# Optimization experiments

Hardware: AMD Instinct MI355X
Metric: run time of the kernel (lower is better)

Reference implementation:

```python
import jax, jax.numpy as jnp
import numpy as np
import math

LMAX = 3
NCHAN = 32
NEDGE = 50000

# ---------- Wigner 3j (real spherical-harmonic basis), replicating e3nn ----------

def _su2_cg(j1, j2, j3):
    f = math.factorial
    def coeff(m1, m2, m3):
        vmin = int(max(-j1 + j2 + m3, -j1 + m1, 0))
        vmax = int(min(j2 + j3 + m1, j3 - j1 + j2, j3 + m3))
        C = ((2 * j3 + 1) * f(j3 + j1 - j2) * f(j3 - j1 + j2) * f(j1 + j2 - j3) / f(j1 + j2 + j3 + 1)) ** 0.5
        C *= (f(j3 + m3) * f(j3 - m3) * f(j1 - m1) * f(j1 + m1) * f(j2 - m2) * f(j2 + m2)) ** 0.5
        S = 0.0
        for v in range(vmin, vmax + 1):
            S += (-1.0) ** (v + j2 + m2) * f(j2 + j3 + m1 - v) * f(j1 - m1 + v) / (
                f(v) * f(j3 - j1 + j2 - v) * f(j3 + m3 - v) * f(v + j1 - j2 - m3))
        return C * S
    out = np.zeros((2 * j1 + 1, 2 * j2 + 1, 2 * j3 + 1))
    for m1 in range(-j1, j1 + 1):
        for m2 in range(-j2, j2 + 1):
            m3 = m1 + m2
            if -j3 <= m3 <= j3:
                out[m1 + j1, m2 + j2, m3 + j3] = coeff(m1, m2, m3)
    return out

def _q_real_to_complex(l):
    q = np.zeros((2 * l + 1, 2 * l + 1), dtype=np.complex128)
    for m in range(-l, 0):
        q[l + m, l + abs(m)] = 1 / 2 ** 0.5
        q[l + m, l - abs(m)] = -1j / 2 ** 0.5
    q[l, l] = 1.0
    for m in range(1, l + 1):
        q[l + m, l + abs(m)] = (-1) ** m / 2 ** 0.5
        q[l + m, l - abs(m)] = 1j * (-1) ** m / 2 ** 0.5
    return (-1j) ** l * q

def _wigner_3j(l1, l2, l3):
    C = _su2_cg(l1, l2, l3).astype(np.complex128)
    Q1, Q2, Q3 = _q_real_to_complex(l1), _q_real_to_complex(l2), _q_real_to_complex(l3)
    C = np.einsum('ij,kl,mn,ikn->jlm', Q1, Q2, np.conj(Q3.T), C)
    C = np.real(C)
    return C / np.linalg.norm(C)

# ---------- Instruction enumeration (matches the torch module's __init__) ----------

def _build_paths():
    ls = list(range(LMAX + 1))  # irreps 0e,1o,2e,3o -> parity (-1)^l
    ins = []
    for l1 in ls:
        for l2 in ls:
            for l3 in range(abs(l1 - l2), min(l1 + l2, LMAX) + 1):
                if (l1 + l2 + l3) % 2 == 0:  # parity selection p1*p2 == p3
                    ins.append((l1, l2, l3))
    # e3nn Irreps.sort: stable sort of output blocks by ir; pos[i] = sorted position
    order_sorted = sorted(range(len(ins)), key=lambda i: ins[i][2])
    pos = [0] * len(ins)
    for new, old in enumerate(order_sorted):
        pos[old] = new
    # replicate `outputs.insert(ins.i_out, output)` over instruction iteration order
    concat = []
    for idx in range(len(ins)):
        concat.insert(min(pos[idx], len(concat)), idx)
    offs = np.cumsum([0] + [2 * l + 1 for l in ls]).tolist()  # block offsets in dim-16 layout
    # path_weight: component normalization, one path per output block -> sqrt(2*l3+1)
    cg = [jnp.asarray((_wigner_3j(l1, l2, l3) * math.sqrt(2 * l3 + 1)).astype(np.float32))
          for (l1, l2, l3) in ins]
    return ins, pos, concat, offs, cg

_INS, _POS, _CONCAT, _OFFS, _CG = _build_paths()  # 23 instructions, out dim 99


def setup_inputs() -> dict:
    key = jax.random.key(0)
    k1, k2, k3 = jax.random.split(key, 3)
    x = jax.random.normal(k1, (NEDGE, NCHAN, 16), dtype=jnp.float32)
    y = jax.random.normal(k2, (NEDGE, 1, 16), dtype=jnp.float32)
    weights = jax.random.normal(k3, (NEDGE, len(_INS) * NCHAN, 1), dtype=jnp.float32)
    return {"x": x, "y": y, "weights": weights}


def reference(x, y, weights):
    # x: [E, C, 16], y: [E, 1, 16], weights: [E, n_ins*C, 1]
    C = x.shape[1]
    y2 = y[:, 0, :]  # [E, 16]
    outs = [None] * len(_INS)
    for idx, (l1, l2, l3) in enumerate(_INS):
        o1, o2 = _OFFS[l1], _OFFS[l2]
        xb = x[:, :, o1:o1 + 2 * l1 + 1]            # [E, C, 2l1+1]
        yb = y2[:, o2:o2 + 2 * l2 + 1]              # [E, 2l2+1]
        w = weights[:, _POS[idx] * C:(_POS[idx] + 1) * C, 0]  # [E, C]
        # dense CG contraction == sparse gather-multiply-index_add over (mu1,mu2,mu3)
        blk = jnp.einsum('eci,ej,ijk->eck', xb, yb, _CG[idx])  # [E, C, 2l3+1]
        outs[idx] = w[:, :, None] * blk
    return jnp.concatenate([outs[i] for i in _CONCAT], axis=-1)  # [E, C, 99]
```

## Files before the change

kernel.cpp:

```cpp
#include <hip/hip_runtime.h>
#include <math.h>

#define NPATH 23
#define NEDGE 50000
#define NCHAN 32
#define NWROW 736
#define OUTW  99
#define TTOT  439
#define EPB   2
#define NTHR  256

constexpr int L1[NPATH]    = {0,0,0,0,1,1,1,1,1,1,2,2,2,2,2,2,2,3,3,3,3,3,3};
constexpr int L2[NPATH]    = {0,1,2,3,0,1,1,2,2,3,0,1,1,2,2,3,3,0,1,2,2,3,3};
constexpr int L3[NPATH]    = {0,1,2,3,1,0,2,1,3,2,2,1,3,0,2,1,3,3,2,1,3,0,2};
constexpr int POS[NPATH]   = {0,4,10,17,5,1,11,6,18,12,13,7,19,2,14,8,20,21,15,9,22,3,16};
constexpr int OOFF[NPATH]  = {0,4,7,12,19,1,34,22,39,46,51,31,61,2,73,25,78,85,68,28,92,3,56};
constexpr int TOFF[NPATH]  = {0,1,4,9,16,25,28,43,52,73,88,113,128,163,168,193,208,243,292,327,348,397,404};
constexpr int LOFF[4]      = {0,1,4,9};

constexpr unsigned GMASK4[4] = {0xE0010u, 0x700100u, 0x7C00u, 0x182EFu};

typedef _Float16 __attribute__((ext_vector_type(4))) h4;

__device__ __forceinline__ int imx(int a, int b){ return a > b ? a : b; }
__device__ __forceinline__ int imn(int a, int b){ return a < b ? a : b; }

__device__ __forceinline__ double factd(int n){
    double r = 1.0;
    for(int i = 2; i <= n; ++i) r *= (double)i;
    return r;
}

__global__ __launch_bounds__(512) void cg_setup(float* __restrict__ cgd2){
    const int p  = blockIdx.x;
    const int j1 = L1[p], j2 = L2[p], j3 = L3[p];
    const int n1 = 2*j1+1, n2 = 2*j2+1, n3 = 2*j3+1;
    const int o2 = LOFF[j2];
    const int ntot = n1*n2*n3;
    const int t = threadIdx.x;

    __shared__ double scg[343];
    __shared__ double qre[3][49];
    __shared__ double qim[3][49];
    __shared__ double red[512];

    if(t < ntot){
        int a   = t / (n2*n3);
        int rem = t - a*(n2*n3);
        int b   = rem / n3;
        int g   = rem - b*n3;
        int m1 = a - j1, m2 = b - j2, m3 = g - j3;
        double val = 0.0;
        if(m1 + m2 == m3){
            int vmin = imx(imx(-j1 + j2 + m3, -j1 + m1), 0);
            int vmax = imn(imn(j2 + j3 + m1, j3 - j1 + j2), j3 + m3);
            double C = sqrt((2.0*j3 + 1.0) * factd(j3 + j1 - j2) * factd(j3 - j1 + j2)
                            * factd(j1 + j2 - j3) / factd(j1 + j2 + j3 + 1));
            C *= sqrt(factd(j3 + m3) * factd(j3 - m3) * factd(j1 - m1)
                      * factd(j1 + m1) * factd(j2 - m2) * factd(j2 + m2));
            double S = 0.0;
            for(int v = vmin; v <= vmax; ++v){
                double sgn = ((v + j2 + m2) & 1) ? -1.0 : 1.0;
                S += sgn * factd(j2 + j3 + m1 - v) * factd(j1 - m1 + v)
                     / (factd(v) * factd(j3 - j1 + j2 - v) * factd(j3 + m3 - v)
                        * factd(v + j1 - j2 - m3));
            }
            val = C * S;
        }
        scg[t] = val;
    }

    if(t < 3){
        int l = (t == 0) ? j1 : ((t == 1) ? j2 : j3);
        int n = 2*l + 1;
        double* QR = qre[t];
        double* QI = qim[t];
        for(int i = 0; i < 49; ++i){ QR[i] = 0.0; QI[i] = 0.0; }
        const double is2 = 0.70710678118654752440;
        for(int m = -l; m < 0; ++m){
            QR[(l+m)*n + (l-m)] = is2;
            QI[(l+m)*n + (l+m)] = -is2;
        }
        QR[l*n + l] = 1.0;
        for(int m = 1; m <= l; ++m){
            double s = (m & 1) ? -1.0 : 1.0;
            QR[(l+m)*n + (l+m)] = s * is2;
            QI[(l+m)*n + (l-m)] = s * is2;
        }
        double fr, fi;
        switch(l & 3){
            case 0: fr = 1.0;  fi = 0.0;  break;
            case 1: fr = 0.0;  fi = -1.0; break;
            case 2: fr = -1.0; fi = 0.0;  break;
            default: fr = 0.0; fi = 1.0;  break;
        }
        for(int i = 0; i < n*n; ++i){
            double re = QR[i], im = QI[i];
            QR[i] = re*fr - im*fi;
            QI[i] = re*fi + im*fr;
        }
    }
    __syncthreads();

    double val = 0.0;
    if(t < ntot){
        int j   = t / (n2*n3);
        int rem = t - j*(n2*n3);
        int lq  = rem / n3;
        int m   = rem - lq*n3;
        double acc = 0.0;
        for(int i = 0; i < n1; ++i){
            double q1r = qre[0][i*n1 + j], q1i = qim[0][i*n1 + j];
            if(q1r == 0.0 && q1i == 0.0) continue;
            for(int k = 0; k < n2; ++k){
                double q2r = qre[1][k*n2 + lq], q2i = qim[1][k*n2 + lq];
                if(q2r == 0.0 && q2i == 0.0) continue;
                double ar = q1r*q2r - q1i*q2i;
                double ai = q1r*q2i + q1i*q2r;
                for(int n = 0; n < n3; ++n){
                    double cv = scg[(i*n2 + k)*n3 + n];
                    if(cv == 0.0) continue;
                    double q3r = qre[2][n*n3 + m];
                    double q3i = -qim[2][n*n3 + m];
                    acc += cv * (ar*q3r - ai*q3i);
                }
            }
        }
        val = acc;
    }

    red[t] = val * val;
    __syncthreads();
    if(t < 343) scg[t] = val;
    for(int s2 = 256; s2 > 0; s2 >>= 1){
        if(t < s2) red[t] += red[t + s2];
        __syncthreads();
    }
    const double scale = sqrt(2.0*j3 + 1.0) / sqrt(red[0]);

    for(int u = t; u < n1*n3*16; u += 512){
        int sl = u >> 4, jf = u & 15;
        int i  = sl / n3, k = sl - i*n3;
        int j  = jf - o2;
        double v2 = (j >= 0 && j < n2) ? scg[(i*n2 + j)*n3 + k] : 0.0;
        cgd2[(size_t)(TOFF[p] + sl)*16 + jf] = (float)(v2 * scale);
    }
}

template<int G>
__device__ __forceinline__ void prefetchW(const float* __restrict__ wbase,
                                          float* __restrict__ wreg)
{
    constexpr unsigned mask = GMASK4[G];
    #pragma unroll
    for(int p = 0; p < NPATH; ++p){
        if((mask >> p) & 1u)
            wreg[__builtin_popcount(mask & ((1u << p) - 1u))] = wbase[POS[p]*NCHAN];
    }
}

template<int G>
__device__ __forceinline__ void phaseC(const float* __restrict__ xr,
                                       const float* __restrict__ wreg,
                                       const float* __restrict__ Te,
                                       _Float16* __restrict__ ob)
{
    constexpr unsigned mask = GMASK4[G];
    #pragma unroll
    for(int p = 0; p < NPATH; ++p){
        if(!((mask >> p) & 1u)) continue;
        const int widx = __builtin_popcount(mask & ((1u << p) - 1u));
        const int n1 = 2*L1[p] + 1;
        const int n3 = 2*L3[p] + 1;
        const int o1 = LOFF[L1[p]];
        const float wp = wreg[widx];
        const float* Tp = Te + TOFF[p];
        #pragma unroll
        for(int k = 0; k < n3; ++k){
            float acc = 0.f;
            #pragma unroll
            for(int i = 0; i < n1; ++i)
                acc = fmaf(xr[o1 + i], Tp[i*n3 + k], acc);
            ob[OOFF[p] + k] = (_Float16)(wp * acc);
        }
    }
}

__global__ __launch_bounds__(NTHR, 6) void tp_main(
    const float* __restrict__ x, const float* __restrict__ y,
    const float* __restrict__ w, const float* __restrict__ cgd2,
    float* __restrict__ out)
{
    __shared__ __align__(16) _Float16 obuf[EPB*NCHAN*OUTW];
    __shared__ float Ts[EPB*TTOT];
    __shared__ float ys[EPB*16];

    const int tid = threadIdx.x;
    const int e0  = blockIdx.x * EPB;

    const int c   = tid & 31;
    const int el  = (tid >> 5) & 1;
    const int grp = tid >> 6;
    const int e   = e0 + el;

    const float4* xp = reinterpret_cast<const float4*>(x + (size_t)(e*NCHAN + c)*16);
    float4 x0 = xp[0], x1 = xp[1], x2 = xp[2], x3 = xp[3];

    const float* wbase = w + (size_t)e*NWROW + c;
    float wreg[10];
    switch(grp){
        case 0: prefetchW<0>(wbase, wreg); break;
        case 1: prefetchW<1>(wbase, wreg); break;
        case 2: prefetchW<2>(wbase, wreg); break;
        default: prefetchW<3>(wbase, wreg); break;
    }

    if(tid < EPB*16) ys[tid] = y[e0*16 + tid];
    __syncthreads();

    for(int u = tid; u < EPB*TTOT; u += NTHR){
        int eli = u / TTOT;
        int s   = u - eli*TTOT;
        const float* cr = cgd2 + (size_t)s*16;
        float acc = 0.f;
        #pragma unroll
        for(int j = 0; j < 16; ++j)
            acc = fmaf(ys[eli*16 + j], cr[j], acc);
        Ts[u] = acc;
    }
    __syncthreads();

    float xr[16];
    xr[0]=x0.x;  xr[1]=x0.y;  xr[2]=x0.z;  xr[3]=x0.w;
    xr[4]=x1.x;  xr[5]=x1.y;  xr[6]=x1.z;  xr[7]=x1.w;
    xr[8]=x2.x;  xr[9]=x2.y;  xr[10]=x2.z; xr[11]=x2.w;
    xr[12]=x3.x; xr[13]=x3.y; xr[14]=x3.z; xr[15]=x3.w;

    const float* Te = Ts + el*TTOT;
    _Float16* ob = obuf + el*(NCHAN*OUTW) + c*OUTW;

    switch(grp){
        case 0: phaseC<0>(xr, wreg, Te, ob); break;
        case 1: phaseC<1>(xr, wreg, Te, ob); break;
        case 2: phaseC<2>(xr, wreg, Te, ob); break;
        default: phaseC<3>(xr, wreg, Te, ob); break;
    }
    __syncthreads();

    const h4* ob4 = reinterpret_cast<const h4*>(obuf);
    float4* o4 = reinterpret_cast<float4*>(out + (size_t)blockIdx.x * (EPB*NCHAN*OUTW));
    #pragma unroll
    for(int k2 = 0; k2 < 7; ++k2){
        int idx = tid + k2*NTHR;
        if(idx < EPB*NCHAN*OUTW/4){
            h4 hv = ob4[idx];
            float4 fv = { (float)hv[0], (float)hv[1], (float)hv[2], (float)hv[3] };
            o4[idx] = fv;
        }
    }
}

extern "C" void kernel_launch(void* const* d_in, const int* in_sizes, int n_in,
                              void* d_out, int out_size, void* d_ws, size_t ws_size,
                              hipStream_t stream)
{
    const float* x  = (const float*)d_in[0];
    const float* y  = (const float*)d_in[1];
    const float* wt = (const float*)d_in[2];
    float* out = (float*)d_out;
    float* cgd2 = (float*)d_ws;

    cg_setup<<<NPATH, 512, 0, stream>>>(cgd2);
    tp_main<<<NEDGE/EPB, NTHR, 0, stream>>>(x, y, wt, cgd2, out);
}
```

Before: 267.9 us.

## Compute per-wave CG-y tables locally, pad T layout, pair fp16 LDS stores

Rebalances the path-to-wave grouping so each wave builds only the y-contracted CG entries it will itself consume. That removes the block-wide __syncthreads and the staged y in shared memory, leaving a wave-local lgkmcnt wait. The T table is padded to 4 or 8 floats per row so phase C can read it with float4 LDS loads, and fp16 results are written to LDS in pairs. The obuf row stride is padded to 100. The final global write becomes per-element scalar stores instead of aligned float4 stores, which may reduce store efficiency in a bandwidth-bound kernel.

```diff
diff --git a/kernel.cpp b/kernel.cpp
--- a/kernel.cpp
+++ b/kernel.cpp
@@ -18,7 +18,44 @@
 constexpr int TOFF[NPATH]  = {0,1,4,9,16,25,28,43,52,73,88,113,128,163,168,193,208,243,292,327,348,397,404};
 constexpr int LOFF[4]      = {0,1,4,9};
 
-constexpr unsigned GMASK4[4] = {0xE0010u, 0x700100u, 0x7C00u, 0x182EFu};
+constexpr unsigned GMASKS[4] = {0x122028u, 0x211405u, 0x444100u, 0x88AD2u};
+
+constexpr int PAD(int n1){ return n1 <= 3 ? 4 : 8; }
+
+struct PT { int v[NPATH]; int total; };
+constexpr PT make_ptoff(){
+    PT t{}; int a = 0;
+    for(int p = 0; p < NPATH; ++p){ t.v[p] = a; a += (2*L3[p]+1)*PAD(2*L1[p]+1); }
+    t.total = a;
+    return t;
+}
+constexpr PT PTOF = make_ptoff();
+static_assert(PTOF.total == 632, "padded T size");
+#define TSZ 632
+
+struct BTab { unsigned v[4][28]; int cnt[4]; };
+constexpr BTab make_btab(){
+    BTab b{};
+    for(int g = 0; g < 4; ++g){
+        int n = 0;
+        for(int p = 0; p < NPATH; ++p){
+            if(!((GMASKS[g] >> p) & 1u)) continue;
+            int n1 = 2*L1[p]+1, n3 = 2*L3[p]+1;
+            int o2 = LOFF[L2[p]];
+            int q0 = o2 >> 2;
+            for(int k = 0; k < n3; ++k){
+                b.v[g][n++] = (unsigned)(TOFF[p]+k)
+                            | ((unsigned)n3 << 9) | ((unsigned)n1 << 12)
+                            | ((unsigned)(PAD(n1)==8 ? 1 : 0) << 15)
+                            | ((unsigned)(PTOF.v[p] + k*PAD(n1)) << 16)
+                            | ((unsigned)q0 << 26);
+            }
+        }
+        b.cnt[g] = n;
+    }
+    return b;
+}
+constexpr BTab BT = make_btab();
 
 typedef _Float16 __attribute__((ext_vector_type(4))) h4;
 
@@ -151,11 +188,56 @@
 __device__ __forceinline__ void prefetchW(const float* __restrict__ wbase,
                                           float* __restrict__ wreg)
 {
-    constexpr unsigned mask = GMASK4[G];
+    constexpr unsigned mask = GMASKS[G];
     #pragma unroll
     for(int p = 0; p < NPATH; ++p){
         if((mask >> p) & 1u)
             wreg[__builtin_popcount(mask & ((1u << p) - 1u))] = wbase[POS[p]*NCHAN];
+    }
+}
+
+template<int G>
+__device__ __forceinline__ void phaseB(int lane, int e0,
+                                       const float* __restrict__ y,
+                                       const float* __restrict__ cgd2,
+                                       float* __restrict__ TsL)
+{
+    constexpr int E = BT.cnt[G];
+    if(lane < 2*E){
+        const int el  = (lane >= E) ? 1 : 0;
+        const int idx = lane - el*E;
+        const unsigned ent = BT.v[G][idx];
+        const int slot0 = ent & 511;
+        const int n3    = (ent >> 9)  & 7;
+        const int n1    = (ent >> 12) & 7;
+        const int pad8  = (ent >> 15) & 1;
+        const int dst   = (ent >> 16) & 1023;
+        const int q0    = (ent >> 26) & 3;
+
+        const float* yq = y + (size_t)(e0 + el)*16 + q0*4;
+        float4 y0 = *(const float4*)yq;
+        float4 y1 = *(const float4*)(yq + 4);
+
+        float T[8];
+        #pragma unroll
+        for(int i = 0; i < 8; ++i) T[i] = 0.f;
+        #pragma unroll
+        for(int i = 0; i < 7; ++i){
+            if(i < n1){
+                const float* cr = cgd2 + (size_t)(slot0 + i*n3)*16 + q0*4;
+                float4 c0 = *(const float4*)cr;
+                float4 c1 = *(const float4*)(cr + 4);
+                float a;
+                a = fmaf(c0.x, y0.x, 0.f);  a = fmaf(c0.y, y0.y, a);
+                a = fmaf(c0.z, y0.z, a);    a = fmaf(c0.w, y0.w, a);
+                a = fmaf(c1.x, y1.x, a);    a = fmaf(c1.y, y1.y, a);
+                a = fmaf(c1.z, y1.z, a);    a = fmaf(c1.w, y1.w, a);
+                T[i] = a;
+            }
+        }
+        float* d = TsL + el*TSZ + dst;
+        *(float4*)d = float4{T[0], T[1], T[2], T[3]};
+        if(pad8) *((float4*)d + 1) = float4{T[4], T[5], T[6], T[7]};
     }
 }
 
@@ -165,24 +247,54 @@
                                        const float* __restrict__ Te,
                                        _Float16* __restrict__ ob)
 {
-    constexpr unsigned mask = GMASK4[G];
+    constexpr unsigned mask = GMASKS[G];
     #pragma unroll
     for(int p = 0; p < NPATH; ++p){
         if(!((mask >> p) & 1u)) continue;
         const int widx = __builtin_popcount(mask & ((1u << p) - 1u));
-        const int n1 = 2*L1[p] + 1;
-        const int n3 = 2*L3[p] + 1;
-        const int o1 = LOFF[L1[p]];
+        const int n1  = 2*L1[p] + 1;
+        const int n3  = 2*L3[p] + 1;
+        const int o1  = LOFF[L1[p]];
+        const int pad = PAD(n1);
         const float wp = wreg[widx];
-        const float* Tp = Te + TOFF[p];
+
+        float acc[7];
         #pragma unroll
         for(int k = 0; k < n3; ++k){
-            float acc = 0.f;
-            #pragma unroll
-            for(int i = 0; i < n1; ++i)
-                acc = fmaf(xr[o1 + i], Tp[i*n3 + k], acc);
-            ob[OOFF[p] + k] = (_Float16)(wp * acc);
-        }
+            const float* tr = Te + PTOF.v[p] + k*pad;
+            float4 t0 = *(const float4*)tr;
+            float a = xr[o1] * t0.x;
+            if(n1 > 1){
+                a = fmaf(xr[o1+1], t0.y, a);
+                a = fmaf(xr[o1+2], t0.z, a);
+            }
+            if(n1 > 3){
+                a = fmaf(xr[o1+3], t0.w, a);
+                float4 t1 = *((const float4*)tr + 1);
+                a = fmaf(xr[o1+4], t1.x, a);
+                if(n1 > 5){
+                    a = fmaf(xr[o1+5], t1.y, a);
+                    a = fmaf(xr[o1+6], t1.z, a);
+                }
+            }
+            acc[k] = a * wp;
+        }
+
+        const int off  = OOFF[p];
+        const int lead = off & 1;
+        if(lead) ob[off] = (_Float16)acc[0];
+        const int npair = (n3 - lead) >> 1;
+        #pragma unroll
+        for(int kk = 0; kk < npair; ++kk){
+            const int k0 = lead + 2*kk;
+            _Float16 h0 = (_Float16)acc[k0];
+            _Float16 h1 = (_Float16)acc[k0+1];
+            unsigned u = (unsigned)__builtin_bit_cast(unsigned short, h0)
+                       | ((unsigned)__builtin_bit_cast(unsigned short, h1) << 16);
+            *reinterpret_cast<unsigned*>(
+                reinterpret_cast<char*>(ob) + (size_t)(off + k0)*2) = u;
+        }
+        if((n3 - lead) & 1) ob[off + n3 - 1] = (_Float16)acc[n3-1];
     }
 }
 
@@ -191,17 +303,17 @@
     const float* __restrict__ w, const float* __restrict__ cgd2,
     float* __restrict__ out)
 {
-    __shared__ __align__(16) _Float16 obuf[EPB*NCHAN*OUTW];
-    __shared__ float Ts[EPB*TTOT];
-    __shared__ float ys[EPB*16];
+    __shared__ __align__(16) _Float16 obuf[EPB*NCHAN*100];
+    __shared__ __align__(16) float Ts[EPB*TSZ];
 
     const int tid = threadIdx.x;
     const int e0  = blockIdx.x * EPB;
 
-    const int c   = tid & 31;
-    const int el  = (tid >> 5) & 1;
-    const int grp = tid >> 6;
-    const int e   = e0 + el;
+    const int lane = tid & 63;
+    const int c    = tid & 31;
+    const int el   = (tid >> 5) & 1;
+    const int grp  = tid >> 6;
+    const int e    = e0 + el;
 
     const float4* xp = reinterpret_cast<const float4*>(x + (size_t)(e*NCHAN + c)*16);
     float4 x0 = xp[0], x1 = xp[1], x2 = xp[2], x3 = xp[3];
@@ -215,20 +327,15 @@
         default: prefetchW<3>(wbase, wreg); break;
     }
 
-    if(tid < EPB*16) ys[tid] = y[e0*16 + tid];
-    __syncthreads();
-
-    for(int u = tid; u < EPB*TTOT; u += NTHR){
-        int eli = u / TTOT;
-        int s   = u - eli*TTOT;
-        const float* cr = cgd2 + (size_t)s*16;
-        float acc = 0.f;
-        #pragma unroll
-        for(int j = 0; j < 16; ++j)
-            acc = fmaf(ys[eli*16 + j], cr[j], acc);
-        Ts[u] = acc;
-    }
-    __syncthreads();
+    switch(grp){
+        case 0: phaseB<0>(lane, e0, y, cgd2, Ts); break;
+        case 1: phaseB<1>(lane, e0, y, cgd2, Ts); break;
+        case 2: phaseB<2>(lane, e0, y, cgd2, Ts); break;
+        default: phaseB<3>(lane, e0, y, cgd2, Ts); break;
+    }
+
+    asm volatile("s_waitcnt lgkmcnt(0)" ::: "memory");
+    __builtin_amdgcn_sched_barrier(0);
 
     float xr[16];
     xr[0]=x0.x;  xr[1]=x0.y;  xr[2]=x0.z;  xr[3]=x0.w;
@@ -236,8 +343,8 @@
     xr[8]=x2.x;  xr[9]=x2.y;  xr[10]=x2.z; xr[11]=x2.w;
     xr[12]=x3.x; xr[13]=x3.y; xr[14]=x3.z; xr[15]=x3.w;
 
-    const float* Te = Ts + el*TTOT;
-    _Float16* ob = obuf + el*(NCHAN*OUTW) + c*OUTW;
+    const float* Te = Ts + el*TSZ;
+    _Float16* ob = obuf + (el*NCHAN + c)*100;
 
     switch(grp){
         case 0: phaseC<0>(xr, wreg, Te, ob); break;
@@ -248,15 +355,16 @@
     __syncthreads();
 
     const h4* ob4 = reinterpret_cast<const h4*>(obuf);
-    float4* o4 = reinterpret_cast<float4*>(out + (size_t)blockIdx.x * (EPB*NCHAN*OUTW));
-    #pragma unroll
-    for(int k2 = 0; k2 < 7; ++k2){
-        int idx = tid + k2*NTHR;
-        if(idx < EPB*NCHAN*OUTW/4){
-            h4 hv = ob4[idx];
-            float4 fv = { (float)hv[0], (float)hv[1], (float)hv[2], (float)hv[3] };
-            o4[idx] = fv;
-        }
+    for(int idx = tid; idx < EPB*NCHAN*25; idx += NTHR){
+        int row = idx / 25;
+        int j   = idx - row*25;
+        h4 hv = ob4[idx];
+        float* base = out + (size_t)(e0 + (row >> 5))*(NCHAN*OUTW)
+                          + (size_t)(row & 31)*OUTW + j*4;
+        base[0] = (float)hv[0];
+        base[1] = (float)hv[1];
+        base[2] = (float)hv[2];
+        if(j < 24) base[3] = (float)hv[3];
     }
 }
 
```

Measured after the change: 271.0 us. Within noise of the previous version (+1.2%).
